# Kernel optimization log

Hardware: AMD Instinct MI355X
Metric: run time of the kernel (lower is better)

## Reference

```python
import jax, jax.numpy as jnp
import numpy as np

B, N, H = 4, 200, 300


def setup_inputs() -> dict:
    key = jax.random.key(0)
    ks = jax.random.split(key, 6)
    s = 1.0 / np.sqrt(H)
    return {
        "x": jax.random.normal(ks[0], (B, N, H), dtype=jnp.float32),
        "e": jax.random.normal(ks[1], (B, N, N, H), dtype=jnp.float32),
        "U_w": jax.random.uniform(ks[2], (H, H), jnp.float32, -s, s),
        "U_b": jax.random.uniform(ks[3], (H,), jnp.float32, -s, s),
        "V_w": jax.random.uniform(ks[4], (H, H), jnp.float32, -s, s),
        "V_b": jax.random.uniform(ks[5], (H,), jnp.float32, -s, s),
    }


def reference(x, e, U_w, U_b, V_w, V_b):
    # Ue = e @ U_w.T + U_b  -> (B, N, N, H)
    Ue = jnp.einsum("bijh,gh->bijg", e, U_w) + U_b
    # Vx = x @ V_w.T + V_b  -> (B, N, H)
    Vx = jnp.einsum("bnh,gh->bng", x, V_w) + V_b
    # e_new[b,i,j] = Ue[b,i,j] + Vx[b,i] + Vx[b,j]
    e_new = Ue + Vx[:, :, None, :] + Vx[:, None, :, :]
    return e_new
```

## Files before the change

### kernel.cpp

```cpp
#include <hip/hip_runtime.h>
#include <hip/hip_bf16.h>

#define BB 4
#define NN 200
#define HH 300
#define NCH 10
#define GHF 10
#define BM 64

typedef __attribute__((ext_vector_type(8))) short short8;
typedef __attribute__((ext_vector_type(4))) float float4v;

static __device__ __forceinline__ ushort f2bf(float x) {
    union { float f; uint u; } v; v.f = x;
    uint r = v.u + 0x7FFFu + ((v.u >> 16) & 1u);
    return (ushort)(r >> 16);
}

static __device__ __forceinline__ short8 pack8_cvt(float4v a, float4v b) {
    uint u0, u1, u2, u3;
    asm("v_cvt_pk_bf16_f32 %0, %1, %2" : "=v"(u0) : "v"(a[0]), "v"(a[1]));
    asm("v_cvt_pk_bf16_f32 %0, %1, %2" : "=v"(u1) : "v"(a[2]), "v"(a[3]));
    asm("v_cvt_pk_bf16_f32 %0, %1, %2" : "=v"(u2) : "v"(b[0]), "v"(b[1]));
    asm("v_cvt_pk_bf16_f32 %0, %1, %2" : "=v"(u3) : "v"(b[2]), "v"(b[3]));
    union { uint u[4]; short8 s; } r;
    r.u[0] = u0; r.u[1] = u1; r.u[2] = u2; r.u[3] = u3;
    return r.s;
}

static __device__ __forceinline__ void gload_lds16(const void* g, void* l) {
    __builtin_amdgcn_global_load_lds(
        (const __attribute__((address_space(1))) unsigned int*)g,
        (__attribute__((address_space(3))) unsigned int*)l, 16, 0, 0);
}

__global__ void pack_u(const float* __restrict__ Uw, ushort* __restrict__ Bp) {
    int idx = blockIdx.x * 256 + threadIdx.x;
    if (idx >= 2 * NCH * GHF * 64) return;
    int lane = idx & 63;
    int rem = idx >> 6;
    int fh = rem % GHF;
    int ks = (rem / GHF) % NCH;
    int gh = rem / (GHF * NCH);
    int g = (gh * GHF + fh) * 16 + (lane & 15);
    int h0 = ks * 32 + (lane >> 4) * 8;
    ushort v[8];
#pragma unroll
    for (int j = 0; j < 8; ++j) {
        int h = h0 + j;
        v[j] = (g < HH && h < HH) ? f2bf(Uw[g * HH + h]) : (ushort)0;
    }
    *reinterpret_cast<short8*>(Bp + (size_t)idx * 8) = *reinterpret_cast<const short8*>(v);
}

__global__ void vx_kernel(const float* __restrict__ x, const float* __restrict__ Vw,
                          const float* __restrict__ Vb, const float* __restrict__ Ub,
                          float* __restrict__ Vx) {
    __shared__ float xs[HH];
    int row = blockIdx.x;
    const float* xr = x + (size_t)row * HH;
    for (int h = threadIdx.x; h < HH; h += 256) xs[h] = xr[h];
    __syncthreads();
    for (int g = threadIdx.x; g < HH; g += 256) {
        const float4* wr = reinterpret_cast<const float4*>(Vw + (size_t)g * HH);
        const float4* xv = reinterpret_cast<const float4*>(xs);
        float s0 = 0.f, s1 = 0.f, s2 = 0.f, s3 = 0.f;
#pragma unroll 5
        for (int k = 0; k < HH / 4; ++k) {
            float4 w = wr[k];
            float4 xx = xv[k];
            s0 += w.x * xx.x; s1 += w.y * xx.y; s2 += w.z * xx.z; s3 += w.w * xx.w;
        }
        Vx[(size_t)row * HH + g] = Vb[g] + 0.5f * Ub[g] + s0 + s1 + s2 + s3;
    }
}

__launch_bounds__(256, 5)
__global__ void gemm_kernel(const float* __restrict__ e, const ushort* __restrict__ Bp,
                            const float* __restrict__ Vx, float* __restrict__ out) {
    __shared__ __align__(16) ushort Alds[2][BM * 32];
    __shared__ __align__(16) ushort Blds[2][GHF * 512];
    const int tid = threadIdx.x;
    const int w = tid >> 6, l = tid & 63;
    const int r = l & 15, q = l >> 4;
    const int gh = blockIdx.x & 1;
    const int m0 = (blockIdx.x >> 1) * BM;
    const int arow = tid >> 2;
    const int acg = tid & 3;
    const float* rowp = e + (size_t)(m0 + arow) * HH;
    const int awidx = ((arow >> 4) * 64 + (arow & 15) + acg * 16) * 8;
    const char* bbase = (const char*)Bp + (size_t)gh * (NCH * GHF * 1024);

    float4v s0a, s0b, s1a, s1b, s2a, s2b;

    float4v acc[GHF];
#pragma unroll
    for (int f = 0; f < GHF; ++f) acc[f] = (float4v){0.f, 0.f, 0.f, 0.f};

#define LOAD_A(K_, S_) do {                                                     \
        int c0_ = (K_) * 32 + acg * 8;                                          \
        const float* p0_ = (c0_ + 4 <= HH) ? rowp + c0_ : e;                    \
        const float* p1_ = (c0_ + 8 <= HH) ? rowp + c0_ + 4 : e;                \
        S_##a = *reinterpret_cast<const float4v*>(p0_);                         \
        S_##b = *reinterpret_cast<const float4v*>(p1_);                         \
    } while (0)

#define WRITE_A(K_, S_, P_) do {                                                \
        short8 w_ = pack8_cvt(S_##a, S_##b);                                    \
        if ((K_) == 9) {                                                        \
            _Pragma("unroll")                                                   \
            for (int j_ = 0; j_ < 8; ++j_)                                      \
                if (288 + acg * 8 + j_ >= HH) w_[j_] = 0;                       \
        }                                                                       \
        *reinterpret_cast<short8*>(&Alds[P_][awidx]) = w_;                      \
    } while (0)

#define ISSUE_B(K_, P_) do {                                                    \
        const char* bs_ = bbase + (size_t)(K_) * (GHF * 1024);                  \
        char* bd_ = (char*)&Blds[P_][0];                                        \
        gload_lds16(bs_ + tid * 16,        bd_ + tid * 16);                     \
        gload_lds16(bs_ + 4096 + tid * 16, bd_ + 4096 + tid * 16);              \
        if (tid < 128)                                                          \
            gload_lds16(bs_ + 8192 + tid * 16, bd_ + 8192 + tid * 16);          \
    } while (0)

#define COMPUTE(P_) do {                                                        \
        short8 fa_ = *reinterpret_cast<const short8*>(&Alds[P_][(w * 64 + l) * 8]); \
        const ushort* bb_ = &Blds[P_][l * 8];                                   \
        _Pragma("unroll")                                                       \
        for (int f_ = 0; f_ < GHF; ++f_) {                                      \
            short8 bf_ = *reinterpret_cast<const short8*>(bb_ + f_ * 512);      \
            acc[f_] = __builtin_amdgcn_mfma_f32_16x16x32_bf16(bf_, fa_, acc[f_], 0, 0, 0); \
        }                                                                       \
    } while (0)

#define WAITV(N_) do {                                                          \
        __builtin_amdgcn_sched_barrier(0);                                      \
        asm volatile("s_waitcnt vmcnt(" #N_ ")" ::: "memory");                  \
        __builtin_amdgcn_sched_barrier(0);                                      \
    } while (0)

#define ENDPHASE() do {                                                         \
        asm volatile("s_waitcnt lgkmcnt(0)" ::: "memory");                      \
        __builtin_amdgcn_s_barrier();                                           \
        __builtin_amdgcn_sched_barrier(0);                                      \
    } while (0)

    LOAD_A(0, s0); ISSUE_B(0, 0); LOAD_A(1, s1); LOAD_A(2, s2);
    WRITE_A(0, s0, 0);
    WAITV(2);
    ENDPHASE();

    WRITE_A(1, s1, 1); ISSUE_B(1, 1); LOAD_A(3, s0); COMPUTE(0); WAITV(2); ENDPHASE();
    WRITE_A(2, s2, 0); ISSUE_B(2, 0); LOAD_A(4, s1); COMPUTE(1); WAITV(2); ENDPHASE();
    WRITE_A(3, s0, 1); ISSUE_B(3, 1); LOAD_A(5, s2); COMPUTE(0); WAITV(2); ENDPHASE();
    WRITE_A(4, s1, 0); ISSUE_B(4, 0); LOAD_A(6, s0); COMPUTE(1); WAITV(2); ENDPHASE();
    WRITE_A(5, s2, 1); ISSUE_B(5, 1); LOAD_A(7, s1); COMPUTE(0); WAITV(2); ENDPHASE();
    WRITE_A(6, s0, 0); ISSUE_B(6, 0); LOAD_A(8, s2); COMPUTE(1); WAITV(2); ENDPHASE();
    WRITE_A(7, s1, 1); ISSUE_B(7, 1); LOAD_A(9, s0); COMPUTE(0); WAITV(2); ENDPHASE();
    WRITE_A(8, s2, 0); ISSUE_B(8, 0);                COMPUTE(1); WAITV(0); ENDPHASE();
    WRITE_A(9, s0, 1); ISSUE_B(9, 1);                COMPUTE(0); WAITV(0); ENDPHASE();
    COMPUTE(1);

    {
        const int mrow = m0 + w * 16 + r;
        int j = mrow % NN;
        int ti = mrow / NN;
        int b = ti / NN;
        const float* vi = Vx + (size_t)ti * HH;
        const float* vj = Vx + (size_t)(b * NN + j) * HH;
        float* orow = out + (size_t)mrow * HH;
        const int gbase = gh * (GHF * 16);
#pragma unroll
        for (int f = 0; f < GHF; ++f) {
            int g0 = gbase + f * 16 + q * 4;
            if (g0 + 4 <= HH) {
                float4v vi4 = *reinterpret_cast<const float4v*>(vi + g0);
                float4v vj4 = *reinterpret_cast<const float4v*>(vj + g0);
                *reinterpret_cast<float4v*>(orow + g0) = acc[f] + vi4 + vj4;
            }
        }
    }
#undef LOAD_A
#undef WRITE_A
#undef ISSUE_B
#undef COMPUTE
#undef WAITV
#undef ENDPHASE
}

extern "C" void kernel_launch(void* const* d_in, const int* in_sizes, int n_in,
                              void* d_out, int out_size, void* d_ws, size_t ws_size,
                              hipStream_t stream) {
    const float* x  = (const float*)d_in[0];
    const float* e  = (const float*)d_in[1];
    const float* Uw = (const float*)d_in[2];
    const float* Ub = (const float*)d_in[3];
    const float* Vw = (const float*)d_in[4];
    const float* Vb = (const float*)d_in[5];
    float* out = (float*)d_out;

    ushort* Bp = (ushort*)d_ws;
    float*  Vx = (float*)((char*)d_ws + 204800);

    pack_u<<<50, 256, 0, stream>>>(Uw, Bp);
    vx_kernel<<<BB * NN, 256, 0, stream>>>(x, Vw, Vb, Ub, Vx);
    gemm_kernel<<<5000, 256, 0, stream>>>(e, Bp, Vx, out);
}
```

Measured before the change: 185.0 us.

## Restructure GEMM pipeline to prefetch B two stages ahead with two A register sets

Result: no change. 185.7 us (+0.4%).

```diff
diff --git a/kernel.cpp b/kernel.cpp
--- a/kernel.cpp
+++ b/kernel.cpp
@@ -32,6 +32,11 @@
     __builtin_amdgcn_global_load_lds(
         (const __attribute__((address_space(1))) unsigned int*)g,
         (__attribute__((address_space(3))) unsigned int*)l, 16, 0, 0);
+}
+static __device__ __forceinline__ void gload_lds4(const void* g, void* l) {
+    __builtin_amdgcn_global_load_lds(
+        (const __attribute__((address_space(1))) unsigned int*)g,
+        (__attribute__((address_space(3))) unsigned int*)l, 4, 0, 0);
 }
 
 __global__ void pack_u(const float* __restrict__ Uw, ushort* __restrict__ Bp) {
@@ -75,7 +80,7 @@
     }
 }
 
-__launch_bounds__(256, 5)
+__launch_bounds__(256, 4)
 __global__ void gemm_kernel(const float* __restrict__ e, const ushort* __restrict__ Bp,
                             const float* __restrict__ Vx, float* __restrict__ out) {
     __shared__ __align__(16) ushort Alds[2][BM * 32];
@@ -91,7 +96,7 @@
     const int awidx = ((arow >> 4) * 64 + (arow & 15) + acg * 16) * 8;
     const char* bbase = (const char*)Bp + (size_t)gh * (NCH * GHF * 1024);
 
-    float4v s0a, s0b, s1a, s1b, s2a, s2b;
+    float4v s0a, s0b, s1a, s1b;
 
     float4v acc[GHF];
 #pragma unroll
@@ -120,8 +125,8 @@
         char* bd_ = (char*)&Blds[P_][0];                                        \
         gload_lds16(bs_ + tid * 16,        bd_ + tid * 16);                     \
         gload_lds16(bs_ + 4096 + tid * 16, bd_ + 4096 + tid * 16);              \
-        if (tid < 128)                                                          \
-            gload_lds16(bs_ + 8192 + tid * 16, bd_ + 8192 + tid * 16);          \
+        gload_lds4(bs_ + 8192 + w * 512 + l * 4,       bd_ + 8192 + w * 512 + l * 4); \
+        gload_lds4(bs_ + 8448 + w * 512 + l * 4,       bd_ + 8448 + w * 512 + l * 4); \
     } while (0)
 
 #define COMPUTE(P_) do {                                                        \
@@ -140,26 +145,36 @@
         __builtin_amdgcn_sched_barrier(0);                                      \
     } while (0)
 
-#define ENDPHASE() do {                                                         \
+#define BARX() do {                                                             \
         asm volatile("s_waitcnt lgkmcnt(0)" ::: "memory");                      \
         __builtin_amdgcn_s_barrier();                                           \
         __builtin_amdgcn_sched_barrier(0);                                      \
     } while (0)
 
-    LOAD_A(0, s0); ISSUE_B(0, 0); LOAD_A(1, s1); LOAD_A(2, s2);
+    LOAD_A(0, s0); ISSUE_B(0, 0);
+    LOAD_A(1, s1); ISSUE_B(1, 1);
     WRITE_A(0, s0, 0);
-    WAITV(2);
-    ENDPHASE();
-
-    WRITE_A(1, s1, 1); ISSUE_B(1, 1); LOAD_A(3, s0); COMPUTE(0); WAITV(2); ENDPHASE();
-    WRITE_A(2, s2, 0); ISSUE_B(2, 0); LOAD_A(4, s1); COMPUTE(1); WAITV(2); ENDPHASE();
-    WRITE_A(3, s0, 1); ISSUE_B(3, 1); LOAD_A(5, s2); COMPUTE(0); WAITV(2); ENDPHASE();
-    WRITE_A(4, s1, 0); ISSUE_B(4, 0); LOAD_A(6, s0); COMPUTE(1); WAITV(2); ENDPHASE();
-    WRITE_A(5, s2, 1); ISSUE_B(5, 1); LOAD_A(7, s1); COMPUTE(0); WAITV(2); ENDPHASE();
-    WRITE_A(6, s0, 0); ISSUE_B(6, 0); LOAD_A(8, s2); COMPUTE(1); WAITV(2); ENDPHASE();
-    WRITE_A(7, s1, 1); ISSUE_B(7, 1); LOAD_A(9, s0); COMPUTE(0); WAITV(2); ENDPHASE();
-    WRITE_A(8, s2, 0); ISSUE_B(8, 0);                COMPUTE(1); WAITV(0); ENDPHASE();
-    WRITE_A(9, s0, 1); ISSUE_B(9, 1);                COMPUTE(0); WAITV(0); ENDPHASE();
+    WAITV(6); BARX();
+
+#define PHASE(I_, PC_, PN_, SLD_, SWR_) do {                                    \
+        COMPUTE(PC_); BARX();                                                   \
+        ISSUE_B((I_) + 2, PC_); LOAD_A((I_) + 2, SLD_);                         \
+        WRITE_A((I_) + 1, SWR_, PN_);                                           \
+        WAITV(6); BARX();                                                       \
+    } while (0)
+
+    PHASE(0, 0, 1, s0, s1);
+    PHASE(1, 1, 0, s1, s0);
+    PHASE(2, 0, 1, s0, s1);
+    PHASE(3, 1, 0, s1, s0);
+    PHASE(4, 0, 1, s0, s1);
+    PHASE(5, 1, 0, s1, s0);
+    PHASE(6, 0, 1, s0, s1);
+    PHASE(7, 1, 0, s1, s0);
+
+    COMPUTE(0); BARX();
+    WRITE_A(9, s1, 1);
+    WAITV(0); BARX();
     COMPUTE(1);
 
     {
@@ -186,7 +201,8 @@
 #undef ISSUE_B
 #undef COMPUTE
 #undef WAITV
-#undef ENDPHASE
+#undef BARX
+#undef PHASE
 }
 
 extern "C" void kernel_launch(void* const* d_in, const int* in_sizes, int n_in,
```
